# Kernel optimization log

Hardware: AMD Instinct MI355X
Metric: run time of the kernel (lower is better)

The kernel has to match this reference:

```python
import jax, jax.numpy as jnp
import numpy as np

N = 50000      # nodes
HID = 128      # hidden_dim
E = 1600000    # edges per sparse operator (avg degree 32)


def _spmm(rows, cols, vals, x):
    # y = A @ x for COO sparse A: gather source rows, scale, scatter-add to dest rows
    return jax.ops.segment_sum(vals[:, None] * x[cols], rows, num_segments=N)


def setup_inputs() -> dict:
    key = jax.random.key(0)
    ks = jax.random.split(key, 22)

    def edges(i):
        return (jax.random.randint(ks[i], (E,), 0, N, dtype=jnp.int64) if jax.config.jax_enable_x64 else jax.random.randint(ks[i], (E,), 0, N).astype(jnp.int32),
                jax.random.randint(ks[i + 1], (E,), 0, N).astype(jnp.int32),
                jax.random.uniform(ks[i + 2], (E,), jnp.float32))

    A_rows, A_cols, A_vals = edges(0)
    P1_rows, P1_cols, P1_vals = edges(3)
    P2_rows, P2_cols, P2_vals = edges(6)
    P3_rows, P3_cols, P3_vals = edges(9)
    Ps_rows, Ps_cols, Ps_vals = edges(12)

    X = jax.random.normal(ks[15], (N, HID), jnp.float32)
    a = jax.random.normal(ks[16], (2 * HID, 1), jnp.float32) * 0.1
    W1 = jax.random.normal(ks[17], (HID, HID), jnp.float32) / jnp.sqrt(HID)
    b1 = jnp.zeros((HID,), jnp.float32)
    W2 = jax.random.normal(ks[18], (HID, HID), jnp.float32) / jnp.sqrt(HID)
    b2 = jnp.zeros((HID,), jnp.float32)

    return dict(X=X, a=a, W1=W1, b1=b1, W2=W2, b2=b2,
                A_rows=A_rows, A_cols=A_cols, A_vals=A_vals,
                P1_rows=P1_rows, P1_cols=P1_cols, P1_vals=P1_vals,
                P2_rows=P2_rows, P2_cols=P2_cols, P2_vals=P2_vals,
                P3_rows=P3_rows, P3_cols=P3_cols, P3_vals=P3_vals,
                Psct_rows=Ps_rows, Psct_cols=Ps_cols, Psct_vals=Ps_vals)


def reference(X, a, W1, b1, W2, b2,
              A_rows, A_cols, A_vals,
              P1_rows, P1_cols, P1_vals,
              P2_rows, P2_cols, P2_vals,
              P3_rows, P3_cols, P3_vals,
              Psct_rows, Psct_cols, Psct_vals):
    h = X  # [N, HID]
    h_A = _spmm(A_rows, A_cols, A_vals, h)
    h_A2 = _spmm(A_rows, A_cols, A_vals, h_A)
    h_A3 = _spmm(A_rows, A_cols, A_vals, h_A2)
    # moment = 1 => |P x| ** 1
    h_s1 = jnp.abs(_spmm(P1_rows, P1_cols, P1_vals, h))
    h_s2 = jnp.abs(_spmm(P2_rows, P2_cols, P2_vals, h))
    h_s3 = jnp.abs(_spmm(P3_rows, P3_cols, P3_vals, h))

    # Faithful to torch: cat along dim 0 then view(N, -1, 2*hid) (row-interleaved layout)
    def pair(hb):
        return jnp.concatenate([h, hb], axis=0).reshape(N, 1, 2 * HID)

    a_input = jnp.concatenate(
        [pair(h_A), pair(h_A2), pair(h_A3), pair(h_s1), pair(h_s2), pair(h_s3)],
        axis=1)  # [N, 6, 2*HID]

    e = jnp.squeeze(jax.nn.relu(a_input) @ a, axis=2)          # [N, 6]
    attention = jax.nn.softmax(e, axis=1).reshape(N, 6, 1)     # [N, 6, 1]

    # Faithful to torch: cat along dim 2 -> [N, HID, 6], then view(N, 6, -1)
    h_all = jnp.concatenate(
        [h_A[:, :, None], h_A2[:, :, None], h_A3[:, :, None],
         h_s1[:, :, None], h_s2[:, :, None], h_s3[:, :, None]],
        axis=2).reshape(N, 6, HID)

    h_prime = jnp.mean(attention * h_all, axis=1)              # [N, HID]

    # Withgres=False: skip gres smoothing (P_sct unused)
    out = jax.nn.leaky_relu(h_prime @ W1.T + b1)               # slope 0.01, matches torch default
    out = jax.nn.leaky_relu(out @ W2.T + b2)
    return out
```

## Files before the change

### kernel.cpp

```cpp
#include <hip/hip_runtime.h>
#include <hip/hip_fp16.h>

#define N_NODES 50000
#define HID 128
#define NE 1600000
#define NH (N_NODES * HID)

#define EPB   4096
#define NBLK1 391
#define NBUK  391
#define TBL   (NBUK * NBLK1)
#define SB    ((TBL + 255) / 256)
#define PTRW  (N_NODES + 2)

typedef _Float16 f16x8 __attribute__((ext_vector_type(8)));
typedef float    f32x4 __attribute__((ext_vector_type(4)));

__device__ __forceinline__ float h2f(unsigned short u) {
    __half_raw r; r.x = u;
    __half h = r;
    return __half2float(h);
}
__device__ __forceinline__ unsigned short f2h(float f) {
    __half h = __float2half_rn(f);
    __half_raw r = h;
    return r.x;
}

__global__ __launch_bounds__(256) void k1_hist4(
    const int* __restrict__ r0, const int* __restrict__ r1,
    const int* __restrict__ r2, const int* __restrict__ r3,
    int* __restrict__ table4, unsigned short* __restrict__ rank4)
{
    __shared__ int h[NBUK];
    int o = blockIdx.y, b = blockIdx.x, t = threadIdx.x;
    const int* rows = o == 0 ? r0 : o == 1 ? r1 : o == 2 ? r2 : r3;
    int* table = table4 + (size_t)o * TBL;
    unsigned short* rank = rank4 + (size_t)o * NE;

    for (int i = t; i < NBUK; i += 256) h[i] = 0;
    __syncthreads();
    int e0 = b * EPB;
    int e1 = min(e0 + EPB, NE);
    for (int e = e0 + t; e < e1; e += 256)
        rank[e] = (unsigned short)atomicAdd(&h[rows[e] >> 7], 1);
    __syncthreads();
    for (int i = t; i < NBUK; i += 256) table[i * NBLK1 + b] = h[i];
}

__global__ __launch_bounds__(256) void s1_partial4(
    const int* __restrict__ table4, int* __restrict__ part4)
{
    __shared__ int red[256];
    int o = blockIdx.y, b = blockIdx.x, t = threadIdx.x;
    const int* table = table4 + (size_t)o * TBL;
    int idx = b * 256 + t;
    red[t] = (idx < TBL) ? table[idx] : 0;
    __syncthreads();
    #pragma unroll
    for (int s = 128; s > 0; s >>= 1) {
        if (t < s) red[t] += red[t + s];
        __syncthreads();
    }
    if (t == 0) part4[o * SB + b] = red[0];
}

__global__ __launch_bounds__(1024) void s2_scan4(int* __restrict__ part4)
{
    __shared__ int sh[1024];
    int o = blockIdx.x, t = threadIdx.x;
    int* part = part4 + o * SB;
    sh[t] = (t < SB) ? part[t] : 0;
    __syncthreads();
    for (int off = 1; off < 1024; off <<= 1) {
        int v = (t >= off) ? sh[t - off] : 0;
        __syncthreads();
        sh[t] += v;
        __syncthreads();
    }
    if (t < SB) part[t] = (t == 0) ? 0 : sh[t - 1];
}

__global__ __launch_bounds__(256) void s3_add4(
    int* __restrict__ table4, const int* __restrict__ part4)
{
    __shared__ int sh[256];
    int o = blockIdx.y, b = blockIdx.x, t = threadIdx.x;
    int* table = table4 + (size_t)o * TBL;
    int idx = b * 256 + t;
    int v = (idx < TBL) ? table[idx] : 0;
    sh[t] = v;
    __syncthreads();
    #pragma unroll
    for (int off = 1; off < 256; off <<= 1) {
        int u = (t >= off) ? sh[t - off] : 0;
        __syncthreads();
        sh[t] += u;
        __syncthreads();
    }
    int excl = (t == 0) ? 0 : sh[t - 1];
    if (idx < TBL) table[idx] = part4[o * SB + b] + excl;
}

__global__ __launch_bounds__(256) void k3_scatter(
    const int* __restrict__ rows, const int* __restrict__ cols,
    const float* __restrict__ vals, const unsigned short* __restrict__ rank,
    const int* __restrict__ table, int2* __restrict__ tmp)
{
    __shared__ int base[NBUK];
    int b = blockIdx.x, t = threadIdx.x;
    for (int i = t; i < NBUK; i += 256) base[i] = table[i * NBLK1 + b];
    __syncthreads();
    int e0 = b * EPB;
    int e1 = min(e0 + EPB, NE);
    for (int e = e0 + t; e < e1; e += 256) {
        int r = rows[e];
        int pos = base[r >> 7] + (int)rank[e];
        tmp[pos] = make_int2(((r & 127) << 16) | cols[e], __float_as_int(vals[e]));
    }
}

__global__ __launch_bounds__(256) void k4_fine(
    const int* __restrict__ table, const int2* __restrict__ tmp,
    int2* __restrict__ pairs, int* __restrict__ rowptr)
{
    __shared__ int cnt[128];
    __shared__ int sh[256];
    __shared__ int nxt[128];
    int k = blockIdx.x, t = threadIdx.x;
    if (t < 128) cnt[t] = 0;
    __syncthreads();
    int base = table[k * NBLK1];
    int end  = (k == NBUK - 1) ? NE : table[(k + 1) * NBLK1];
    for (int e = base + t; e < end; e += 256)
        atomicAdd(&cnt[(tmp[e].x >> 16) & 127], 1);
    __syncthreads();
    sh[t] = (t < 128) ? cnt[t] : 0;
    __syncthreads();
    #pragma unroll
    for (int off = 1; off < 256; off <<= 1) {
        int v = (t >= off) ? sh[t - off] : 0;
        __syncthreads();
        sh[t] += v;
        __syncthreads();
    }
    if (t < 128) {
        int excl = (t == 0) ? 0 : sh[t - 1];
        nxt[t] = base + excl;
        int row = k * 128 + t;
        if (row < N_NODES) rowptr[row] = base + excl;
    }
    if (k == NBUK - 1 && t == 255) rowptr[N_NODES] = NE;
    __syncthreads();
    for (int e = base + t; e < end; e += 256) {
        int2 p = tmp[e];
        int pos = atomicAdd(&nxt[(p.x >> 16) & 127], 1);
        pairs[pos] = make_int2(p.x & 0xFFFF, p.y);
    }
}

__global__ __launch_bounds__(256) void cvt_f2h_kernel(
    const float* __restrict__ in, unsigned short* __restrict__ out, int n4)
{
    int i = blockIdx.x * 256 + threadIdx.x;
    if (i >= n4) return;
    float4 v = ((const float4*)in)[i];
    ushort4 o;
    o.x = f2h(v.x); o.y = f2h(v.y); o.z = f2h(v.z); o.w = f2h(v.w);
    ((ushort4*)out)[i] = o;
}

__device__ __forceinline__ void spmm_row(
    const unsigned short* __restrict__ xh, const int2* __restrict__ pairs,
    int start, int end, int sub, bool do_abs,
    unsigned short* __restrict__ yrow)
{
    const ushort4* x4 = (const ushort4*)xh + sub;

    float4 a0 = {0,0,0,0}, a1 = {0,0,0,0};
    float4 a2 = {0,0,0,0}, a3 = {0,0,0,0};

    #define EDGE_H(P, A) { \
        ushort4 _x = x4[(size_t)(P).x * 32]; \
        float _v = __int_as_float((P).y); \
        A.x += _v * h2f(_x.x); \
        A.y += _v * h2f(_x.y); \
        A.z += _v * h2f(_x.z); \
        A.w += _v * h2f(_x.w); }

    int e = start;
    for (; e + 3 < end; e += 4) {
        int2 p0 = pairs[e];
        int2 p1 = pairs[e + 1];
        int2 p2 = pairs[e + 2];
        int2 p3 = pairs[e + 3];
        EDGE_H(p0, a0); EDGE_H(p1, a1); EDGE_H(p2, a2); EDGE_H(p3, a3);
    }
    for (; e < end; ++e) {
        int2 p0 = pairs[e];
        EDGE_H(p0, a0);
    }
    #undef EDGE_H

    float4 acc;
    acc.x = (a0.x + a1.x) + (a2.x + a3.x);
    acc.y = (a0.y + a1.y) + (a2.y + a3.y);
    acc.z = (a0.z + a1.z) + (a2.z + a3.z);
    acc.w = (a0.w + a1.w) + (a2.w + a3.w);
    if (do_abs) {
        acc.x = fabsf(acc.x); acc.y = fabsf(acc.y);
        acc.z = fabsf(acc.z); acc.w = fabsf(acc.w);
    }
    ushort4 o;
    o.x = f2h(acc.x); o.y = f2h(acc.y); o.z = f2h(acc.z); o.w = f2h(acc.w);
    ((ushort4*)yrow)[sub] = o;
}

__global__ __launch_bounds__(256) void spmm4_kernel(
    const int* __restrict__ ptr4, const int2* __restrict__ pairs4,
    const unsigned short* __restrict__ Xh, unsigned short* __restrict__ B16)
{
    int bid = blockIdx.x;
    int op  = bid & 3;
    int rb  = bid >> 2;
    int r   = rb * 8 + (threadIdx.x >> 5);
    int sub = threadIdx.x & 31;
    if (r >= N_NODES) return;

    const int*  ptr   = ptr4 + (size_t)op * PTRW;
    const int2* pairs = pairs4 + (size_t)op * NE;
    int dst = op ? op + 2 : 0;
    unsigned short* yrow = B16 + (size_t)dst * NH + (size_t)r * HID;

    spmm_row(Xh, pairs, ptr[r], ptr[r + 1], sub, op != 0, yrow);
}

__global__ __launch_bounds__(256) void spmm_chain_kernel(
    const int* __restrict__ ptr, const int2* __restrict__ pairs,
    const unsigned short* __restrict__ src16, unsigned short* __restrict__ dst16)
{
    int t   = blockIdx.x * 256 + threadIdx.x;
    int r   = t >> 5;
    int sub = t & 31;
    if (r >= N_NODES) return;
    spmm_row(src16, pairs, ptr[r], ptr[r + 1], sub, false,
             dst16 + (size_t)r * HID);
}

__global__ __launch_bounds__(256) void attn_kernel(
    const float* __restrict__ X, const unsigned short* __restrict__ B16,
    const float* __restrict__ a, float* __restrict__ att)
{
    int wid  = (blockIdx.x * 256 + threadIdx.x) >> 6;
    int lane = threadIdx.x & 63;
    if (wid >= N_NODES) return;

    const float4 av = ((const float4*)a)[lane];
    float e[6];

    if (wid < N_NODES / 2) {
        const float4 p = ((const float4*)(X + (size_t)wid * 256))[lane];
        float s = fmaxf(p.x, 0.f) * av.x + fmaxf(p.y, 0.f) * av.y +
                  fmaxf(p.z, 0.f) * av.z + fmaxf(p.w, 0.f) * av.w;
        #pragma unroll
        for (int m = 1; m < 64; m <<= 1) s += __shfl_xor(s, m);
        #pragma unroll
        for (int b = 0; b < 6; ++b) e[b] = s;
    } else {
        int m = 2 * wid - N_NODES;
        #pragma unroll
        for (int b = 0; b < 6; ++b) {
            ushort4 u = ((const ushort4*)(B16 + (size_t)b * NH +
                                          (size_t)m * HID))[lane];
            float s = fmaxf(h2f(u.x), 0.f) * av.x + fmaxf(h2f(u.y), 0.f) * av.y +
                      fmaxf(h2f(u.z), 0.f) * av.z + fmaxf(h2f(u.w), 0.f) * av.w;
            #pragma unroll
            for (int k = 1; k < 64; k <<= 1) s += __shfl_xor(s, k);
            e[b] = s;
        }
    }

    if (lane == 0) {
        float mx = e[0];
        #pragma unroll
        for (int b = 1; b < 6; ++b) mx = fmaxf(mx, e[b]);
        float ex[6], sum = 0.f;
        #pragma unroll
        for (int b = 0; b < 6; ++b) { ex[b] = expf(e[b] - mx); sum += ex[b]; }
        float inv = 1.f / sum;
        #pragma unroll
        for (int b = 0; b < 6; ++b) att[(size_t)wid * 6 + b] = ex[b] * inv;
    }
}

__global__ __launch_bounds__(256) void hprime_kernel(
    const unsigned short* __restrict__ B16, const float* __restrict__ att,
    unsigned short* __restrict__ hp16)
{
    int idx = blockIdx.x * 256 + threadIdx.x;
    if (idx >= NH) return;
    int n = idx >> 7;
    int q = idx & 127;
    float s = 0.f;
    #pragma unroll
    for (int p = 0; p < 6; ++p) {
        int f = p * HID + q;
        int j = f % 6;
        int i = f / 6;
        s += att[(size_t)n * 6 + p] *
             h2f(B16[(size_t)j * NH + (size_t)n * HID + i]);
    }
    hp16[idx] = f2h(s * (1.0f / 6.0f));
}

template <bool OUT16>
__global__ __launch_bounds__(256) void fc_mfma_kernel(
    const unsigned short* __restrict__ Ah,
    const unsigned short* __restrict__ Wh,
    const float* __restrict__ bias,
    void* __restrict__ outp)
{
    const int wid  = blockIdx.x * 4 + (threadIdx.x >> 6);
    const int lane = threadIdx.x & 63;
    const int cb   = wid & 7;
    const int o    = cb * 16 + (lane & 15);
    const int kg   = lane >> 4;
    const int nw   = (gridDim.x * 4) >> 3;

    f16x8 bfrag[4];
    #pragma unroll
    for (int ks = 0; ks < 4; ++ks)
        bfrag[ks] = *(const f16x8*)(Wh + (size_t)o * HID + ks * 32 + kg * 8);
    const float bo = bias[o];

    for (int tile = wid >> 3; tile < N_NODES / 16; tile += nw) {
        const int n0 = tile * 16;
        const unsigned short* ar =
            Ah + (size_t)(n0 + (lane & 15)) * HID + kg * 8;
        f32x4 acc = {0.f, 0.f, 0.f, 0.f};
        #pragma unroll
        for (int ks = 0; ks < 4; ++ks) {
            f16x8 af = *(const f16x8*)(ar + ks * 32);
            acc = __builtin_amdgcn_mfma_f32_16x16x32_f16(af, bfrag[ks], acc,
                                                         0, 0, 0);
        }
        #pragma unroll
        for (int j = 0; j < 4; ++j) {
            float v = acc[j] + bo;
            v = v > 0.f ? v : 0.01f * v;
            int n = n0 + kg * 4 + j;
            if (OUT16)
                ((unsigned short*)outp)[(size_t)n * HID + o] = f2h(v);
            else
                ((float*)outp)[(size_t)n * HID + o] = v;
        }
    }
}

extern "C" void kernel_launch(void* const* d_in, const int* in_sizes, int n_in,
                              void* d_out, int out_size, void* d_ws, size_t ws_size,
                              hipStream_t stream)
{
    const float* X  = (const float*)d_in[0];
    const float* a  = (const float*)d_in[1];
    const float* W1 = (const float*)d_in[2];
    const float* b1 = (const float*)d_in[3];
    const float* W2 = (const float*)d_in[4];
    const float* b2 = (const float*)d_in[5];
    const int*   op_rows[4] = { (const int*)d_in[6],  (const int*)d_in[9],
                                (const int*)d_in[12], (const int*)d_in[15] };
    const int*   op_cols[4] = { (const int*)d_in[7],  (const int*)d_in[10],
                                (const int*)d_in[13], (const int*)d_in[16] };
    const float* op_vals[4] = { (const float*)d_in[8],  (const float*)d_in[11],
                                (const float*)d_in[14], (const float*)d_in[17] };

    float* ws = (float*)d_ws;
    size_t off = 0;
    unsigned short* B16 = (unsigned short*)(ws + off);  off += (size_t)6 * NH / 2;
    float* att = ws + off;                              off += (size_t)6 * N_NODES;
    unsigned short* Xh  = (unsigned short*)(ws + off);  off += NH / 2;
    unsigned short* Wh1 = (unsigned short*)(ws + off);  off += HID * HID / 2;
    unsigned short* Wh2 = (unsigned short*)(ws + off);  off += HID * HID / 2;
    int*   ptr4   = (int*)(ws + off);                   off += (size_t)4 * PTRW;
    int*   table4 = (int*)(ws + off);                   off += (size_t)4 * TBL;
    int*   part4  = (int*)(ws + off);                   off += 4 * SB + 8;
    unsigned short* rank4 = (unsigned short*)(ws + off); off += (size_t)4 * NE / 2;
    off = (off + 3) & ~(size_t)3;
    int2*  tmp    = (int2*)(ws + off);                  off += (size_t)2 * NE;
    int2*  pairs4 = (int2*)(ws + off);                  off += (size_t)8 * NE;
    unsigned short* hp16  = (unsigned short*)tmp;
    unsigned short* mid16 = (unsigned short*)pairs4;

    dim3 blk(256);
    const int rg = (N_NODES * 32 + 255) / 256;
    const int cg = (NH / 4 + 255) / 256;
    const int wg = (HID * HID / 4 + 255) / 256;

    cvt_f2h_kernel<<<cg, blk, 0, stream>>>(X, Xh, NH / 4);
    cvt_f2h_kernel<<<wg, blk, 0, stream>>>(W1, Wh1, HID * HID / 4);
    cvt_f2h_kernel<<<wg, blk, 0, stream>>>(W2, Wh2, HID * HID / 4);

    k1_hist4<<<dim3(NBLK1, 4), blk, 0, stream>>>(
        op_rows[0], op_rows[1], op_rows[2], op_rows[3], table4, rank4);
    s1_partial4<<<dim3(SB, 4), blk, 0, stream>>>(table4, part4);
    s2_scan4<<<4, 1024, 0, stream>>>(part4);
    s3_add4<<<dim3(SB, 4), blk, 0, stream>>>(table4, part4);

    for (int o = 0; o < 4; ++o) {
        k3_scatter<<<NBLK1, blk, 0, stream>>>(
            op_rows[o], op_cols[o], op_vals[o],
            rank4 + (size_t)o * NE, table4 + (size_t)o * TBL, tmp);
        k4_fine<<<NBUK, blk, 0, stream>>>(
            table4 + (size_t)o * TBL, tmp,
            pairs4 + (size_t)o * NE, ptr4 + (size_t)o * PTRW);
    }

    spmm4_kernel<<<rg * 4, blk, 0, stream>>>(ptr4, pairs4, Xh, B16);

    spmm_chain_kernel<<<rg, blk, 0, stream>>>(ptr4, pairs4,
                                              B16 + 0 * (size_t)NH,
                                              B16 + 1 * (size_t)NH);
    spmm_chain_kernel<<<rg, blk, 0, stream>>>(ptr4, pairs4,
                                              B16 + 1 * (size_t)NH,
                                              B16 + 2 * (size_t)NH);

    attn_kernel<<<(N_NODES + 3) / 4, blk, 0, stream>>>(X, B16, a, att);
    hprime_kernel<<<(NH + 255) / 256, blk, 0, stream>>>(B16, att, hp16);
    fc_mfma_kernel<true ><<<1024, blk, 0, stream>>>(hp16,  Wh1, b1, mid16);
    fc_mfma_kernel<false><<<1024, blk, 0, stream>>>(mid16, Wh2, b2, d_out);
}
```

Measured before the change: 635.0 us.

## Pack sparse edges into 32-bit col/fp16 value and batch CSR build across operators

Each sparse edge is now stored as one 32-bit word: a 16-bit column index and the edge value as fp16. This halves the index/value traffic in every SpMM pass and in the CSR build. The per-operator scatter and fine-sort launches are merged into single 2D-grid launches over all four operators, using a larger temp buffer. The coarse histogram blocks are also enlarged to cover 8192 edges each. Storing edge values in fp16 adds rounding error, and the 16-bit column field assumes fewer than 65536 nodes.

```diff
diff --git a/kernel.cpp b/kernel.cpp
--- a/kernel.cpp
+++ b/kernel.cpp
@@ -6,8 +6,8 @@
 #define NE 1600000
 #define NH (N_NODES * HID)
 
-#define EPB   4096
-#define NBLK1 391
+#define EPB   8192
+#define NBLK1 196
 #define NBUK  391
 #define TBL   (NBUK * NBLK1)
 #define SB    ((TBL + 255) / 256)
@@ -102,13 +102,25 @@
     if (idx < TBL) table[idx] = part4[o * SB + b] + excl;
 }
 
-__global__ __launch_bounds__(256) void k3_scatter(
-    const int* __restrict__ rows, const int* __restrict__ cols,
-    const float* __restrict__ vals, const unsigned short* __restrict__ rank,
-    const int* __restrict__ table, int2* __restrict__ tmp)
+__global__ __launch_bounds__(256) void k3_scatter4(
+    const int* __restrict__ r0, const int* __restrict__ r1,
+    const int* __restrict__ r2, const int* __restrict__ r3,
+    const int* __restrict__ c0, const int* __restrict__ c1,
+    const int* __restrict__ c2, const int* __restrict__ c3,
+    const float* __restrict__ v0, const float* __restrict__ v1,
+    const float* __restrict__ v2, const float* __restrict__ v3,
+    const unsigned short* __restrict__ rank4,
+    const int* __restrict__ table4, int2* __restrict__ tmp4)
 {
     __shared__ int base[NBUK];
-    int b = blockIdx.x, t = threadIdx.x;
+    int o = blockIdx.y, b = blockIdx.x, t = threadIdx.x;
+    const int*   rows = o == 0 ? r0 : o == 1 ? r1 : o == 2 ? r2 : r3;
+    const int*   cols = o == 0 ? c0 : o == 1 ? c1 : o == 2 ? c2 : c3;
+    const float* vals = o == 0 ? v0 : o == 1 ? v1 : o == 2 ? v2 : v3;
+    const int* table = table4 + (size_t)o * TBL;
+    const unsigned short* rank = rank4 + (size_t)o * NE;
+    int2* tmp = tmp4 + (size_t)o * NE;
+
     for (int i = t; i < NBUK; i += 256) base[i] = table[i * NBLK1 + b];
     __syncthreads();
     int e0 = b * EPB;
@@ -116,24 +128,30 @@
     for (int e = e0 + t; e < e1; e += 256) {
         int r = rows[e];
         int pos = base[r >> 7] + (int)rank[e];
-        tmp[pos] = make_int2(((r & 127) << 16) | cols[e], __float_as_int(vals[e]));
-    }
-}
-
-__global__ __launch_bounds__(256) void k4_fine(
-    const int* __restrict__ table, const int2* __restrict__ tmp,
-    int2* __restrict__ pairs, int* __restrict__ rowptr)
+        unsigned pk = ((unsigned)cols[e] << 16) | (unsigned)f2h(vals[e]);
+        tmp[pos] = make_int2(r & 127, (int)pk);
+    }
+}
+
+__global__ __launch_bounds__(256) void k4_fine4(
+    const int* __restrict__ table4, const int2* __restrict__ tmp4,
+    unsigned* __restrict__ pairs4, int* __restrict__ ptr4)
 {
     __shared__ int cnt[128];
     __shared__ int sh[256];
     __shared__ int nxt[128];
-    int k = blockIdx.x, t = threadIdx.x;
+    int o = blockIdx.y, k = blockIdx.x, t = threadIdx.x;
+    const int* table = table4 + (size_t)o * TBL;
+    const int2* tmp = tmp4 + (size_t)o * NE;
+    unsigned* pairs = pairs4 + (size_t)o * NE;
+    int* rowptr = ptr4 + (size_t)o * PTRW;
+
     if (t < 128) cnt[t] = 0;
     __syncthreads();
     int base = table[k * NBLK1];
     int end  = (k == NBUK - 1) ? NE : table[(k + 1) * NBLK1];
     for (int e = base + t; e < end; e += 256)
-        atomicAdd(&cnt[(tmp[e].x >> 16) & 127], 1);
+        atomicAdd(&cnt[tmp[e].x], 1);
     __syncthreads();
     sh[t] = (t < 128) ? cnt[t] : 0;
     __syncthreads();
@@ -154,8 +172,8 @@
     __syncthreads();
     for (int e = base + t; e < end; e += 256) {
         int2 p = tmp[e];
-        int pos = atomicAdd(&nxt[(p.x >> 16) & 127], 1);
-        pairs[pos] = make_int2(p.x & 0xFFFF, p.y);
+        int pos = atomicAdd(&nxt[p.x], 1);
+        pairs[pos] = (unsigned)p.y;
     }
 }
 
@@ -171,7 +189,7 @@
 }
 
 __device__ __forceinline__ void spmm_row(
-    const unsigned short* __restrict__ xh, const int2* __restrict__ pairs,
+    const unsigned short* __restrict__ xh, const unsigned* __restrict__ pairs,
     int start, int end, int sub, bool do_abs,
     unsigned short* __restrict__ yrow)
 {
@@ -180,9 +198,10 @@
     float4 a0 = {0,0,0,0}, a1 = {0,0,0,0};
     float4 a2 = {0,0,0,0}, a3 = {0,0,0,0};
 
-    #define EDGE_H(P, A) { \
-        ushort4 _x = x4[(size_t)(P).x * 32]; \
-        float _v = __int_as_float((P).y); \
+    #define EDGE_P(P, A) { \
+        unsigned _p = (P); \
+        float _v = h2f((unsigned short)(_p & 0xFFFFu)); \
+        ushort4 _x = x4[(size_t)(_p >> 16) * 32]; \
         A.x += _v * h2f(_x.x); \
         A.y += _v * h2f(_x.y); \
         A.z += _v * h2f(_x.z); \
@@ -190,17 +209,16 @@
 
     int e = start;
     for (; e + 3 < end; e += 4) {
-        int2 p0 = pairs[e];
-        int2 p1 = pairs[e + 1];
-        int2 p2 = pairs[e + 2];
-        int2 p3 = pairs[e + 3];
-        EDGE_H(p0, a0); EDGE_H(p1, a1); EDGE_H(p2, a2); EDGE_H(p3, a3);
+        unsigned p0 = pairs[e];
+        unsigned p1 = pairs[e + 1];
+        unsigned p2 = pairs[e + 2];
+        unsigned p3 = pairs[e + 3];
+        EDGE_P(p0, a0); EDGE_P(p1, a1); EDGE_P(p2, a2); EDGE_P(p3, a3);
     }
     for (; e < end; ++e) {
-        int2 p0 = pairs[e];
-        EDGE_H(p0, a0);
-    }
-    #undef EDGE_H
+        EDGE_P(pairs[e], a0);
+    }
+    #undef EDGE_P
 
     float4 acc;
     acc.x = (a0.x + a1.x) + (a2.x + a3.x);
@@ -217,7 +235,7 @@
 }
 
 __global__ __launch_bounds__(256) void spmm4_kernel(
-    const int* __restrict__ ptr4, const int2* __restrict__ pairs4,
+    const int* __restrict__ ptr4, const unsigned* __restrict__ pairs4,
     const unsigned short* __restrict__ Xh, unsigned short* __restrict__ B16)
 {
     int bid = blockIdx.x;
@@ -227,8 +245,8 @@
     int sub = threadIdx.x & 31;
     if (r >= N_NODES) return;
 
-    const int*  ptr   = ptr4 + (size_t)op * PTRW;
-    const int2* pairs = pairs4 + (size_t)op * NE;
+    const int*      ptr   = ptr4 + (size_t)op * PTRW;
+    const unsigned* pairs = pairs4 + (size_t)op * NE;
     int dst = op ? op + 2 : 0;
     unsigned short* yrow = B16 + (size_t)dst * NH + (size_t)r * HID;
 
@@ -236,7 +254,7 @@
 }
 
 __global__ __launch_bounds__(256) void spmm_chain_kernel(
-    const int* __restrict__ ptr, const int2* __restrict__ pairs,
+    const int* __restrict__ ptr, const unsigned* __restrict__ pairs,
     const unsigned short* __restrict__ src16, unsigned short* __restrict__ dst16)
 {
     int t   = blockIdx.x * 256 + threadIdx.x;
@@ -386,9 +404,9 @@
     int*   part4  = (int*)(ws + off);                   off += 4 * SB + 8;
     unsigned short* rank4 = (unsigned short*)(ws + off); off += (size_t)4 * NE / 2;
     off = (off + 3) & ~(size_t)3;
-    int2*  tmp    = (int2*)(ws + off);                  off += (size_t)2 * NE;
-    int2*  pairs4 = (int2*)(ws + off);                  off += (size_t)8 * NE;
-    unsigned short* hp16  = (unsigned short*)tmp;
+    int2*     tmp4   = (int2*)(ws + off);               off += (size_t)8 * NE;
+    unsigned* pairs4 = (unsigned*)(ws + off);           off += (size_t)4 * NE;
+    unsigned short* hp16  = (unsigned short*)tmp4;
     unsigned short* mid16 = (unsigned short*)pairs4;
 
     dim3 blk(256);
@@ -405,15 +423,12 @@
     s1_partial4<<<dim3(SB, 4), blk, 0, stream>>>(table4, part4);
     s2_scan4<<<4, 1024, 0, stream>>>(part4);
     s3_add4<<<dim3(SB, 4), blk, 0, stream>>>(table4, part4);
-
-    for (int o = 0; o < 4; ++o) {
-        k3_scatter<<<NBLK1, blk, 0, stream>>>(
-            op_rows[o], op_cols[o], op_vals[o],
-            rank4 + (size_t)o * NE, table4 + (size_t)o * TBL, tmp);
-        k4_fine<<<NBUK, blk, 0, stream>>>(
-            table4 + (size_t)o * TBL, tmp,
-            pairs4 + (size_t)o * NE, ptr4 + (size_t)o * PTRW);
-    }
+    k3_scatter4<<<dim3(NBLK1, 4), blk, 0, stream>>>(
+        op_rows[0], op_rows[1], op_rows[2], op_rows[3],
+        op_cols[0], op_cols[1], op_cols[2], op_cols[3],
+        op_vals[0], op_vals[1], op_vals[2], op_vals[3],
+        rank4, table4, tmp4);
+    k4_fine4<<<dim3(NBUK, 4), blk, 0, stream>>>(table4, tmp4, pairs4, ptr4);
 
     spmm4_kernel<<<rg * 4, blk, 0, stream>>>(ptr4, pairs4, Xh, B16);
 
```

After: 611.5 us. -3.7%, faster.
